# Kernel optimization log

Measured on AMD Instinct MI355X. Metric: run time of the kernel, lower is better.

## Reference

```python
import jax, jax.numpy as jnp
import numpy as np

EPS = 1e-5

def bn(x, gamma, beta, axes):
    # training-mode batchnorm over `axes`, channel axis = 1 (matches nn.BatchNorm1d/2d)
    mean = jnp.mean(x, axis=axes, keepdims=True)
    var = jnp.var(x, axis=axes, keepdims=True)
    shp = [1] * x.ndim
    shp[1] = -1
    return gamma.reshape(shp) * (x - mean) * jax.lax.rsqrt(var + EPS) + beta.reshape(shp)

def setup_inputs():
    key = jax.random.key(0)
    B, N, K, Cin, Cout, m = 4, 4096, 32, 64, 64, 8
    ks = jax.random.split(key, 10)
    def w(k, shape, fan_in):
        return jax.random.normal(k, shape, jnp.float32) * np.float32(np.sqrt(2.0 / fan_in))
    return {
        "x": jax.random.normal(ks[0], (B, Cin, N), jnp.float32),
        "xyz_score": jax.random.normal(ks[1], (B, 66, N, K), jnp.float32),
        "conv1_w": w(ks[2], (Cin, Cin), Cin),
        "bn1_g": jnp.ones((Cin,), jnp.float32), "bn1_b": jnp.zeros((Cin,), jnp.float32),
        "matrice2": w(ks[3], (Cin, m * Cout), Cin),  # weight bank: i x (m*o)
        "sn_w0": w(ks[4], (64, 66), 66), "sn_g0": jnp.ones((64,), jnp.float32), "sn_b0": jnp.zeros((64,), jnp.float32),
        "sn_w1": w(ks[5], (32, 64), 64), "sn_g1": jnp.ones((32,), jnp.float32), "sn_b1": jnp.zeros((32,), jnp.float32),
        "sn_w2": w(ks[6], (16, 32), 32), "sn_g2": jnp.ones((16,), jnp.float32), "sn_b2": jnp.zeros((16,), jnp.float32),
        "sn_w3": w(ks[7], (m, 16), 16), "sn_bias3": jnp.zeros((m,), jnp.float32),
        "bn2_g": jnp.ones((Cout,), jnp.float32), "bn2_b": jnp.zeros((Cout,), jnp.float32),
        "idx": jax.random.randint(ks[8], (B, N, K), 0, N, dtype=jnp.int32),
    }

def reference(x, xyz_score, conv1_w, bn1_g, bn1_b, matrice2,
              sn_w0, sn_g0, sn_b0, sn_w1, sn_g1, sn_b1, sn_w2, sn_g2, sn_b2,
              sn_w3, sn_bias3, bn2_g, bn2_b, idx):
    B, Cin, N = x.shape
    m = sn_w3.shape[0]
    # conv1 (1x1, no bias) + BN1 + ReLU  -> [B, Cin, N]
    h = jnp.einsum('oc,bcn->bon', conv1_w, x)
    h = jax.nn.relu(bn(h, bn1_g, bn1_b, (0, 2)))
    # feat_trans_pointnet: [B,N,Cin] @ [Cin, m*Cout] -> [B,N,m,Cout]
    y = jnp.einsum('bcn,ck->bnk', h, matrice2).reshape(B, N, m, -1)
    # ScoreNet: stack of 1x1 conv2d + BN + ReLU, final conv with bias, softmax over m
    s = xyz_score  # [B, 66, N, K]
    s = jax.nn.relu(bn(jnp.einsum('oc,bcnk->bonk', sn_w0, s), sn_g0, sn_b0, (0, 2, 3)))
    s = jax.nn.relu(bn(jnp.einsum('oc,bcnk->bonk', sn_w1, s), sn_g1, sn_b1, (0, 2, 3)))
    s = jax.nn.relu(bn(jnp.einsum('oc,bcnk->bonk', sn_w2, s), sn_g2, sn_b2, (0, 2, 3)))
    s = jnp.einsum('oc,bcnk->bonk', sn_w3, s) + sn_bias3[None, :, None, None]
    score = jax.nn.softmax(s, axis=1)            # [B, m, N, K], bias=0
    score = jnp.transpose(score, (0, 2, 3, 1))   # [B, N, K, m]
    # assemble_pointnet: gather neighbor transformed feats and score-weight them
    neigh = y[jnp.arange(B)[:, None, None], idx]             # [B, N, K, m, Cout]
    out = jnp.einsum('bnkm,bnkmo->bon', score, neigh)        # [B, Cout, N]
    return jax.nn.relu(bn(out, bn2_g, bn2_b, (0, 2)))
```

## Files before the change

### kernel.cpp

```cpp
#include <hip/hip_runtime.h>
#include <cstdint>

typedef unsigned short u16;
typedef unsigned int   u32;
typedef __attribute__((ext_vector_type(8))) short short8;
typedef __attribute__((ext_vector_type(4))) float f32x4;

constexpr int CB = 4;
constexpr int CN = 4096;
constexpr int CK = 32;
constexpr int NPTS = CB * CN * CK;
constexpr int NBK  = 131072;
constexpr float EPSV = 1e-5f;

struct __align__(16) Q4 { u32 a, b, c, d; };

static __device__ __forceinline__ u16 f2b(float f) {
  union { float f; u32 u; } v; v.f = f;
  u32 u = v.u;
  return (u16)((u + 0x7FFFu + ((u >> 16) & 1u)) >> 16);
}
static __device__ __forceinline__ float b2f(u16 h) {
  union { u32 u; float f; } v; v.u = ((u32)h) << 16;
  return v.f;
}
static __device__ __forceinline__ u32 pk2(float lo, float hi) {
  return (u32)f2b(lo) | ((u32)f2b(hi) << 16);
}
static __device__ __forceinline__ short8 mk8(u32 a, u32 b, u32 c, u32 d) {
  union { u32 w[4]; short8 v; } u; u.w[0]=a; u.w[1]=b; u.w[2]=c; u.w[3]=d; return u.v;
}

__global__ __launch_bounds__(256) void k_conv1(const float* __restrict__ x,
                                               const float* __restrict__ w,
                                               float* __restrict__ h,
                                               float* S, float* Q) {
  __shared__ float wl[64 * 64];
  __shared__ float ls[128];
  int tid = threadIdx.x;
  for (int i = tid; i < 4096; i += 256) wl[i] = w[i];
  if (tid < 128) ls[tid] = 0.f;
  __syncthreads();
  int col = blockIdx.x * 256 + tid;
  int b = col >> 12, n = col & 4095;
  float xr[64];
  const float* xp = x + (size_t)(b * 64) * CN + n;
  #pragma unroll
  for (int c = 0; c < 64; ++c) xr[c] = xp[(size_t)c * CN];
  int lane = tid & 63;
  for (int o = 0; o < 64; ++o) {
    float acc = 0.f;
    const float* wr = &wl[o * 64];
    #pragma unroll
    for (int c = 0; c < 64; ++c) acc = fmaf(wr[c], xr[c], acc);
    h[(size_t)(b * 64 + o) * CN + n] = acc;
    float v = acc, v2 = acc * acc;
    for (int d = 1; d < 64; d <<= 1) { v += __shfl_xor(v, d); v2 += __shfl_xor(v2, d); }
    if (lane == 0) { atomicAdd(&ls[o], v); atomicAdd(&ls[64 + o], v2); }
  }
  __syncthreads();
  if (tid < 64) atomicAdd(&S[tid], ls[tid]);
  else if (tid < 128) atomicAdd(&Q[tid - 64], ls[tid]);
}

__global__ __launch_bounds__(64) void k_affine(const float* S, const float* Q,
                                               const float* g, const float* bt,
                                               float* A, float* Bo, int C, float inv_cnt) {
  int t = threadIdx.x;
  if (t < C) {
    float mean = S[t] * inv_cnt;
    float var = fmaxf(Q[t] * inv_cnt - mean * mean, 0.f);
    float a = g[t] * rsqrtf(var + EPSV);
    A[t] = a;
    Bo[t] = bt[t] - mean * a;
  }
}

__global__ __launch_bounds__(256) void k_y(const float* __restrict__ h,
                                           const float* __restrict__ M2,
                                           const float* __restrict__ Ah,
                                           const float* __restrict__ Bh,
                                           u16* __restrict__ y16) {
  __shared__ float at[64 * 16];
  __shared__ float m2[64 * 128];
  int tid = threadIdx.x;
  int blk = blockIdx.x;
  int b = blk >> 8;
  int n0 = (blk & 255) * 16;
  for (int v = tid; v < 1024; v += 256) {
    int c = v >> 4, nn = v & 15;
    float hv = h[(size_t)(b * 64 + c) * CN + n0 + nn];
    at[v] = fmaxf(fmaf(Ah[c], hv, Bh[c]), 0.f);
  }
  int nn = tid >> 4, k8 = tid & 15;
  for (int ch = 0; ch < 4; ++ch) {
    __syncthreads();
    for (int v = tid; v < 8192; v += 256) {
      int c = v >> 7, kk = v & 127;
      m2[v] = M2[c * 512 + ch * 128 + kk];
    }
    __syncthreads();
    float acc[8] = {0, 0, 0, 0, 0, 0, 0, 0};
    for (int c = 0; c < 64; ++c) {
      float av = at[c * 16 + nn];
      const float* mp = &m2[c * 128 + k8 * 8];
      #pragma unroll
      for (int j = 0; j < 8; ++j) acc[j] = fmaf(av, mp[j], acc[j]);
    }
    u16* yp = &y16[((size_t)(b * CN + n0 + nn)) * 512 + ch * 128 + k8 * 8];
    *(short8*)yp = mk8(pk2(acc[0], acc[1]), pk2(acc[2], acc[3]),
                       pk2(acc[4], acc[5]), pk2(acc[6], acc[7]));
  }
}

static __device__ __forceinline__ void ld_frags(const float* __restrict__ xyz,
                                                int c, int g, int pl, short8 fr[5]) {
  int pbase = c * 32;
  int b = pbase >> 17, r = pbase & (NBK - 1);
  const float* base = xyz + (size_t)b * 66 * NBK + r + g * 8;
  #pragma unroll
  for (int ci = 0; ci < 4; ++ci) {
    const float* p = base + (size_t)(16 * ci + pl) * NBK;
    float4 v0 = *(const float4*)p;
    float4 v1 = *(const float4*)(p + 4);
    fr[ci] = mk8(pk2(v0.x, v0.y), pk2(v0.z, v0.w), pk2(v1.x, v1.y), pk2(v1.z, v1.w));
  }
  if (pl < 2) {
    const float* p = base + (size_t)(64 + pl) * NBK;
    float4 v0 = *(const float4*)p;
    float4 v1 = *(const float4*)(p + 4);
    fr[4] = mk8(pk2(v0.x, v0.y), pk2(v0.z, v0.w), pk2(v1.x, v1.y), pk2(v1.z, v1.w));
  } else if (pl == 2) {
    fr[4] = mk8(0x3F803F80u, 0x3F803F80u, 0x3F803F80u, 0x3F803F80u);
  } else {
    fr[4] = mk8(0u, 0u, 0u, 0u);
  }
}

__global__ __launch_bounds__(256) void k_moment(const float* __restrict__ xyz,
                                                float* __restrict__ Mpart) {
  constexpr int TI[15] = {0,0,0,0,0,1,1,1,1,2,2,2,3,3,4};
  constexpr int TJ[15] = {0,1,2,3,4,1,2,3,4,2,3,4,3,4,4};
  int tid = threadIdx.x;
  int wv = tid >> 6;
  int wid = blockIdx.x * 4 + wv;
  int lane = tid & 63, g = lane >> 4, pl = lane & 15;
  f32x4 acc[15];
  #pragma unroll
  for (int t = 0; t < 15; ++t) acc[t] = (f32x4){0.f, 0.f, 0.f, 0.f};
  for (int cc = wid; cc < NPTS / 32; cc += 4096) {
    short8 fr0[5], fr1[5];
    ld_frags(xyz, cc,        g, pl, fr0);
    ld_frags(xyz, cc + 2048, g, pl, fr1);
    #pragma unroll
    for (int t = 0; t < 15; ++t)
      acc[t] = __builtin_amdgcn_mfma_f32_16x16x32_bf16(fr0[TI[t]], fr0[TJ[t]], acc[t], 0, 0, 0);
    #pragma unroll
    for (int t = 0; t < 15; ++t)
      acc[t] = __builtin_amdgcn_mfma_f32_16x16x32_bf16(fr1[TI[t]], fr1[TJ[t]], acc[t], 0, 0, 0);
  }
  float* mp = Mpart + (size_t)wid * 3840;
  #pragma unroll
  for (int t = 0; t < 15; ++t)
    *(f32x4*)(mp + t * 256 + lane * 4) = acc[t];
}

__global__ __launch_bounds__(256) void k_mreduce(const float* __restrict__ Mpart,
                                                 float* __restrict__ M) {
  int e = blockIdx.x * 256 + threadIdx.x;
  int kg = blockIdx.y;
  float s = 0.f;
  for (int k = kg * 256; k < kg * 256 + 256; ++k) s += Mpart[(size_t)k * 3840 + e];
  atomicAdd(&M[e], s);
}

__global__ __launch_bounds__(256) void k_affine1m(const float* __restrict__ M,
                                                  const float* __restrict__ w0,
                                                  const float* __restrict__ g0,
                                                  const float* __restrict__ b0,
                                                  float* __restrict__ A1,
                                                  float* __restrict__ B1) {
  __shared__ float lsM[67 * 68];
  __shared__ float w0l[64 * 69];
  __shared__ float red[4 * 64];
  int tid = threadIdx.x;
  const float inv = 1.f / (float)NPTS;
  for (int i = tid; i < 67 * 67; i += 256) {
    int r = i / 67, c = i % 67;
    int rr = r, cc = c;
    if ((r >> 4) > (c >> 4)) { rr = c; cc = r; }
    int ti = rr >> 4, tj = cc >> 4;
    int t = ti * (9 - ti) / 2 + tj;
    int rho = rr & 15, kap = cc & 15;
    lsM[r * 68 + c] = M[t * 256 + ((rho >> 2) * 16 + kap) * 4 + (rho & 3)] * inv;
  }
  for (int i = tid; i < 64 * 66; i += 256) {
    int o = i / 66, c = i % 66;
    w0l[o * 69 + c] = w0[i];
  }
  __syncthreads();
  int o = tid & 63, sl = tid >> 6;
  float acc2 = 0.f;
  for (int c1 = sl * 17; c1 < sl * 17 + 17; ++c1) {
    if (c1 >= 66) break;
    float inner = 0.f;
    const float* mr = &lsM[c1 * 68];
    const float* wr = &w0l[o * 69];
    for (int c2 = 0; c2 < 66; ++c2) inner = fmaf(mr[c2], wr[c2], inner);
    acc2 = fmaf(wr[c1], inner, acc2);
  }
  red[sl * 64 + o] = acc2;
  __syncthreads();
  if (sl == 0) {
    float Ez2 = red[o] + red[64 + o] + red[128 + o] + red[192 + o];
    float mean = 0.f;
    const float* wr = &w0l[o * 69];
    for (int c = 0; c < 66; ++c) mean = fmaf(wr[c], lsM[c * 68 + 66], mean);
    float var = fmaxf(Ez2 - mean * mean, 0.f);
    float a = g0[o] * rsqrtf(var + EPSV);
    A1[o] = a;
    B1[o] = b0[o] - mean * a;
  }
}

__global__ __launch_bounds__(256) void k_prep(const float* __restrict__ w0,
                                              const float* __restrict__ w1,
                                              const float* __restrict__ A1,
                                              const float* __restrict__ B1,
                                              u16* __restrict__ w0frag,
                                              u16* __restrict__ w1frag) {
  int tid = threadIdx.x;
  for (int i = tid; i < 6144; i += 256) {
    int e = i & 7, lane = (i >> 3) & 63, t = i >> 9;
    int mt = t / 3, kc = t % 3;
    int row = 16 * mt + (lane & 15);
    int k = 32 * kc + 8 * (lane >> 4) + e;
    float v;
    if (k < 66)      v = A1[row] * w0[row * 66 + k];
    else if (k == 66) v = B1[row];
    else              v = 0.f;
    w0frag[i] = f2b(v);
  }
  for (int i = tid; i < 2048; i += 256) {
    int e = i & 7, lane = (i >> 3) & 63, t = i >> 9;
    int m2t = t >> 1, kc2 = t & 1;
    int row = 16 * m2t + (lane & 15);
    int k = 32 * kc2 + 8 * (lane >> 4) + e;
    w1frag[i] = f2b(w1[row * 64 + k]);
  }
}

__global__ __launch_bounds__(256) void k_s2(const float* __restrict__ xyz,
                                            const u16* __restrict__ w0frag,
                                            const u16* __restrict__ w1frag,
                                            u32* __restrict__ z2p,
                                            float* S, float* Q) {
  __shared__ u16 a1l[4][16][80];
  __shared__ float ls2[64];
  int tid = threadIdx.x;
  int wv = tid >> 6, lane = tid & 63, g = lane >> 4, pl = lane & 15;
  if (tid < 64) ls2[tid] = 0.f;
  __syncthreads();

  const short8* w0f = (const short8*)w0frag;
  const short8* w1f = (const short8*)w1frag;
  short8 A0[4][3];
  #pragma unroll
  for (int mt = 0; mt < 4; ++mt)
    #pragma unroll
    for (int kc = 0; kc < 3; ++kc) A0[mt][kc] = w0f[(mt * 3 + kc) * 64 + lane];
  short8 W1f[2][2];
  #pragma unroll
  for (int m2t = 0; m2t < 2; ++m2t)
    #pragma unroll
    for (int kc2 = 0; kc2 < 2; ++kc2) W1f[m2t][kc2] = w1f[(m2t * 2 + kc2) * 64 + lane];

  float sum8[8], sq8[8];
  #pragma unroll
  for (int i = 0; i < 8; ++i) { sum8[i] = 0.f; sq8[i] = 0.f; }

  int wid = blockIdx.x * 4 + wv;
  for (int s = wid; s < NPTS / 16; s += 8192) {
    int pg = s * 16;
    int b = pg >> 17, r = pg & (NBK - 1);
    const float* sb = xyz + (size_t)b * 66 * NBK + r + pl;
    float v[16];
    #pragma unroll
    for (int e = 0; e < 8; ++e) v[e]     = sb[(size_t)(8 * g + e) * NBK];
    #pragma unroll
    for (int e = 0; e < 8; ++e) v[8 + e] = sb[(size_t)(32 + 8 * g + e) * NBK];
    u32 c2a = 0u, c2b = 0u;
    if (g == 0) {
      float v64 = sb[(size_t)64 * NBK];
      float v65 = sb[(size_t)65 * NBK];
      c2a = pk2(v64, v65);
      c2b = 0x00003F80u;
    }
    short8 Bf0 = mk8(pk2(v[0], v[1]), pk2(v[2], v[3]), pk2(v[4], v[5]), pk2(v[6], v[7]));
    short8 Bf1 = mk8(pk2(v[8], v[9]), pk2(v[10], v[11]), pk2(v[12], v[13]), pk2(v[14], v[15]));
    short8 Bf2 = mk8(c2a, c2b, 0u, 0u);

    #pragma unroll
    for (int mt = 0; mt < 4; ++mt) {
      f32x4 z = {0.f, 0.f, 0.f, 0.f};
      z = __builtin_amdgcn_mfma_f32_16x16x32_bf16(A0[mt][0], Bf0, z, 0, 0, 0);
      z = __builtin_amdgcn_mfma_f32_16x16x32_bf16(A0[mt][1], Bf1, z, 0, 0, 0);
      z = __builtin_amdgcn_mfma_f32_16x16x32_bf16(A0[mt][2], Bf2, z, 0, 0, 0);
      float r0 = fmaxf(z[0], 0.f), r1 = fmaxf(z[1], 0.f);
      float r2 = fmaxf(z[2], 0.f), r3 = fmaxf(z[3], 0.f);
      u32* wp = (u32*)&a1l[wv][pl][16 * mt + 4 * g];
      wp[0] = pk2(r0, r1);
      wp[1] = pk2(r2, r3);
    }
    short8 B2f0 = *(const short8*)&a1l[wv][pl][8 * g];
    short8 B2f1 = *(const short8*)&a1l[wv][pl][32 + 8 * g];
    #pragma unroll
    for (int m2t = 0; m2t < 2; ++m2t) {
      f32x4 z2 = {0.f, 0.f, 0.f, 0.f};
      z2 = __builtin_amdgcn_mfma_f32_16x16x32_bf16(W1f[m2t][0], B2f0, z2, 0, 0, 0);
      z2 = __builtin_amdgcn_mfma_f32_16x16x32_bf16(W1f[m2t][1], B2f1, z2, 0, 0, 0);
      #pragma unroll
      for (int rr = 0; rr < 4; ++rr) {
        sum8[m2t * 4 + rr] += z2[rr];
        sq8[m2t * 4 + rr] += z2[rr] * z2[rr];
      }
      int jlo = 8 * m2t + 2 * g;
      z2p[(size_t)jlo * NPTS + pg + pl]       = pk2(z2[0], z2[1]);
      z2p[(size_t)(jlo + 1) * NPTS + pg + pl] = pk2(z2[2], z2[3]);
    }
  }
  #pragma unroll
  for (int i = 0; i < 8; ++i) {
    float vS = sum8[i], vQ = sq8[i];
    for (int d = 1; d < 16; d <<= 1) { vS += __shfl_xor(vS, d); vQ += __shfl_xor(vQ, d); }
    if (pl == 0) {
      int ch = 16 * (i >> 2) + 4 * g + (i & 3);
      atomicAdd(&ls2[ch], vS);
      atomicAdd(&ls2[32 + ch], vQ);
    }
  }
  __syncthreads();
  if (tid < 32) atomicAdd(&S[tid], ls2[tid]);
  else if (tid < 64) atomicAdd(&Q[tid - 32], ls2[tid]);
}

__global__ __launch_bounds__(256) void k_s3(const u32* __restrict__ z2p,
                                            const float* __restrict__ w2,
                                            const float* __restrict__ A2,
                                            const float* __restrict__ B2,
                                            u32* __restrict__ z3,
                                            float* S, float* Q) {
  __shared__ float w2l[16 * 32];
  __shared__ float ab[64];
  __shared__ float ls[32];
  int tid = threadIdx.x;
  for (int i = tid; i < 512; i += 256) w2l[i] = w2[i];
  if (tid < 32) { ab[tid] = A2[tid]; ls[tid] = 0.f; }
  else if (tid < 64) ab[tid] = B2[tid - 32];
  __syncthreads();
  int p = blockIdx.x * 256 + tid;
  float a2[32];
  #pragma unroll
  for (int j = 0; j < 16; ++j) {
    u32 wj = z2p[(size_t)j * NPTS + p];
    float lo = b2f((u16)(wj & 0xFFFFu));
    float hi = b2f((u16)(wj >> 16));
    a2[2 * j]     = fmaxf(fmaf(ab[2 * j], lo, ab[32 + 2 * j]), 0.f);
    a2[2 * j + 1] = fmaxf(fmaf(ab[2 * j + 1], hi, ab[32 + 2 * j + 1]), 0.f);
  }
  int lane = tid & 63;
  float zt[16];
  for (int j = 0; j < 16; ++j) {
    float z = 0.f;
    const float* wr = &w2l[j * 32];
    #pragma unroll
    for (int c = 0; c < 32; ++c) z = fmaf(wr[c], a2[c], z);
    zt[j] = z;
    float v = z, v2 = z * z;
    for (int d = 1; d < 64; d <<= 1) { v += __shfl_xor(v, d); v2 += __shfl_xor(v2, d); }
    if (lane == 0) { atomicAdd(&ls[j], v); atomicAdd(&ls[16 + j], v2); }
  }
  u32 pkk[8];
  #pragma unroll
  for (int j = 0; j < 8; ++j) pkk[j] = pk2(zt[2 * j], zt[2 * j + 1]);
  Q4* dst = (Q4*)(z3 + (size_t)p * 8);
  #pragma unroll
  for (int i = 0; i < 2; ++i) { Q4 q; q.a = pkk[4*i]; q.b = pkk[4*i+1]; q.c = pkk[4*i+2]; q.d = pkk[4*i+3]; dst[i] = q; }
  __syncthreads();
  if (tid < 16) atomicAdd(&S[tid], ls[tid]);
  else if (tid < 32) atomicAdd(&Q[tid - 16], ls[tid]);
}

__global__ __launch_bounds__(256) void k_score(const u32* __restrict__ z3,
                                               const float* __restrict__ w3,
                                               const float* __restrict__ bias3,
                                               const float* __restrict__ A3,
                                               const float* __restrict__ B3,
                                               float* __restrict__ scores) {
  __shared__ float w3l[128];
  __shared__ float bl[8];
  __shared__ float ab[32];
  int tid = threadIdx.x;
  if (tid < 128) w3l[tid] = w3[tid];
  if (tid < 8) bl[tid] = bias3[tid];
  if (tid < 16) ab[tid] = A3[tid];
  else if (tid < 32) ab[tid] = B3[tid - 16];
  __syncthreads();
  int p = blockIdx.x * 256 + tid;
  const Q4* zp = (const Q4*)(z3 + (size_t)p * 8);
  Q4 r0 = zp[0], r1 = zp[1];
  u32 w8[8] = {r0.a, r0.b, r0.c, r0.d, r1.a, r1.b, r1.c, r1.d};
  float a3[16];
  #pragma unroll
  for (int t = 0; t < 8; ++t) {
    int c = t * 2;
    a3[c]     = fmaxf(fmaf(ab[c], b2f((u16)(w8[t] & 0xFFFFu)), ab[16 + c]), 0.f);
    a3[c + 1] = fmaxf(fmaf(ab[c + 1], b2f((u16)(w8[t] >> 16)), ab[16 + c + 1]), 0.f);
  }
  float z4[8]; float mx = -1e30f;
  #pragma unroll
  for (int mI = 0; mI < 8; ++mI) {
    float z = bl[mI];
    const float* wr = &w3l[mI * 16];
    #pragma unroll
    for (int c = 0; c < 16; ++c) z = fmaf(wr[c], a3[c], z);
    z4[mI] = z; mx = fmaxf(mx, z);
  }
  float ssum = 0.f;
  #pragma unroll
  for (int mI = 0; mI < 8; ++mI) { z4[mI] = __expf(z4[mI] - mx); ssum += z4[mI]; }
  float inv = 1.f / ssum;
  float4* sp = (float4*)(scores + (size_t)p * 8);
  sp[0] = make_float4(z4[0] * inv, z4[1] * inv, z4[2] * inv, z4[3] * inv);
  sp[1] = make_float4(z4[4] * inv, z4[5] * inv, z4[6] * inv, z4[7] * inv);
}

__global__ __launch_bounds__(256) void k_gather(const u16* __restrict__ y16,
                                                const float* __restrict__ scores,
                                                const int* __restrict__ idx,
                                                float* __restrict__ out0,
                                                float* S, float* Q) {
  __shared__ float ls[128];
  int tid = threadIdx.x;
  if (tid < 128) ls[tid] = 0.f;
  __syncthreads();
  int bid = blockIdx.x;
  int batch = (bid & 7) >> 1;
  int sub = ((bid >> 3) << 1) | (bid & 1);
  int wv = tid >> 6, lane = tid & 63;
  int m = lane >> 3, og = lane & 7;
  const u16* ybase = y16 + (size_t)batch * CN * 512;
  for (int i = 0; i < 2; ++i) {
    int pid = (batch << 12) + sub * 8 + wv * 2 + i;
    int pbase = pid * 32;
    float acc8[8] = {0, 0, 0, 0, 0, 0, 0, 0};
    for (int k = 0; k < 32; ++k) {
      int p = pbase + k;
      int j = idx[p];
      float s = scores[(size_t)p * 8 + m];
      short8 yv = *(const short8*)(ybase + ((size_t)j << 9) + lane * 8);
      #pragma unroll
      for (int t = 0; t < 8; ++t)
        acc8[t] = fmaf(s, b2f((u16)yv[t]), acc8[t]);
    }
    #pragma unroll
    for (int d = 8; d < 64; d <<= 1) {
      #pragma unroll
      for (int t = 0; t < 8; ++t) acc8[t] += __shfl_xor(acc8[t], d);
    }
    if (m == 0) {
      float* op = out0 + (size_t)pid * 64 + og * 8;
      *(float4*)op       = make_float4(acc8[0], acc8[1], acc8[2], acc8[3]);
      *(float4*)(op + 4) = make_float4(acc8[4], acc8[5], acc8[6], acc8[7]);
      #pragma unroll
      for (int t = 0; t < 8; ++t) {
        atomicAdd(&ls[og * 8 + t], acc8[t]);
        atomicAdd(&ls[64 + og * 8 + t], acc8[t] * acc8[t]);
      }
    }
  }
  __syncthreads();
  if (tid < 64) atomicAdd(&S[tid], ls[tid]);
  else if (tid < 128) atomicAdd(&Q[tid - 64], ls[tid]);
}

__global__ __launch_bounds__(256) void k_bn2(const float* __restrict__ out0,
                                             const float* __restrict__ A,
                                             const float* __restrict__ Bo,
                                             float* __restrict__ outp) {
  int gid = blockIdx.x * 256 + threadIdx.x;
  for (int i = gid; i < CB * 64 * CN; i += 262144) {
    int b = i >> 18, o = (i >> 12) & 63, n = i & 4095;
    float v = out0[((size_t)((b << 12) | n)) * 64 + o];
    outp[i] = fmaxf(fmaf(A[o], v, Bo[o]), 0.f);
  }
}

extern "C" void kernel_launch(void* const* d_in, const int* in_sizes, int n_in,
                              void* d_out, int out_size, void* d_ws, size_t ws_size,
                              hipStream_t stream) {
  const float* x       = (const float*)d_in[0];
  const float* xyz     = (const float*)d_in[1];
  const float* conv1_w = (const float*)d_in[2];
  const float* bn1_g   = (const float*)d_in[3];
  const float* bn1_b   = (const float*)d_in[4];
  const float* M2      = (const float*)d_in[5];
  const float* w0      = (const float*)d_in[6];
  const float* g0      = (const float*)d_in[7];
  const float* b0      = (const float*)d_in[8];
  const float* w1      = (const float*)d_in[9];
  const float* g1      = (const float*)d_in[10];
  const float* b1      = (const float*)d_in[11];
  const float* w2      = (const float*)d_in[12];
  const float* g2      = (const float*)d_in[13];
  const float* b2      = (const float*)d_in[14];
  const float* w3      = (const float*)d_in[15];
  const float* bias3   = (const float*)d_in[16];
  const float* bn2_g   = (const float*)d_in[17];
  const float* bn2_b   = (const float*)d_in[18];
  const int*   idx     = (const int*)d_in[19];
  float* out = (float*)d_out;

  char* wsb = (char*)d_ws;
  float* h      = (float*)wsb;
  u16*   y16    = (u16*)(wsb + 4194304);
  float* scores = (float*)(wsb + 20971520);
  u32*   z2p    = (u32*)(wsb + 37748736);
  u32*   z3     = (u32*)(wsb + 71303168);
  float* out0   = (float*)(wsb + 88080384);
  float* sums   = (float*)(wsb + 92274688);
  float* S_h = sums;        float* Q_h = sums + 64;
  float* S_2 = sums + 128;  float* Q_2 = sums + 160;
  float* S_3 = sums + 192;  float* Q_3 = sums + 208;
  float* S_o = sums + 224;  float* Q_o = sums + 288;
  float* Mm  = sums + 352;
  float* A_h = sums + 6752; float* B_h = sums + 6816;
  float* A_1 = sums + 6880; float* B_1 = sums + 6944;
  float* A_2 = sums + 7008; float* B_2 = sums + 7040;
  float* A_3 = sums + 7072; float* B_3 = sums + 7088;
  float* A_o = sums + 7104; float* B_o = sums + 7168;
  u16* w0frag = (u16*)(sums + 7232);
  u16* w1frag = w0frag + 6144;
  float* Mpart = (float*)z2p;

  hipMemsetAsync(sums, 0, 6752 * sizeof(float), stream);

  k_conv1<<<64, 256, 0, stream>>>(x, conv1_w, h, S_h, Q_h);
  k_affine<<<1, 64, 0, stream>>>(S_h, Q_h, bn1_g, bn1_b, A_h, B_h, 64, 1.f / 16384.f);
  k_y<<<1024, 256, 0, stream>>>(h, M2, A_h, B_h, y16);

  k_moment<<<512, 256, 0, stream>>>(xyz, Mpart);
  k_mreduce<<<dim3(15, 8), 256, 0, stream>>>(Mpart, Mm);
  k_affine1m<<<1, 256, 0, stream>>>(Mm, w0, g0, b0, A_1, B_1);
  k_prep<<<1, 256, 0, stream>>>(w0, w1, A_1, B_1, w0frag, w1frag);
  k_s2<<<2048, 256, 0, stream>>>(xyz, w0frag, w1frag, z2p, S_2, Q_2);
  k_affine<<<1, 64, 0, stream>>>(S_2, Q_2, g1, b1, A_2, B_2, 32, 1.f / (float)NPTS);
  k_s3<<<2048, 256, 0, stream>>>(z2p, w2, A_2, B_2, z3, S_3, Q_3);
  k_affine<<<1, 64, 0, stream>>>(S_3, Q_3, g2, b2, A_3, B_3, 16, 1.f / (float)NPTS);

  k_score<<<2048, 256, 0, stream>>>(z3, w3, bias3, A_3, B_3, scores);
  k_gather<<<2048, 256, 0, stream>>>(y16, scores, idx, out0, S_o, Q_o);
  k_affine<<<1, 64, 0, stream>>>(S_o, Q_o, bn2_g, bn2_b, A_o, B_o, 64, 1.f / 16384.f);
  k_bn2<<<1024, 256, 0, stream>>>(out0, A_o, B_o, out);
}
```

Measured before the change: 379.9 us.

## Compute feature transform y with bf16 MFMA using prepacked M2 fragments

Replaces the scalar-FMA k_y kernel, which reloaded a 64x128 M2 chunk into shared memory four times per block, with a wave-level bf16 MFMA (16x16x32) implementation. A new k_prepM2 kernel converts M2 once into MFMA A-fragment layout in bf16. Each wave computes 16 points x 512 outputs, stages the results in padded LDS and writes them out as coalesced rows. This trades fp32 accumulation of bf16-rounded inputs for matrix-core throughput and adds one small extra launch.

```diff
diff --git a/kernel.cpp b/kernel.cpp
--- a/kernel.cpp
+++ b/kernel.cpp
@@ -76,40 +76,62 @@
   }
 }
 
+__global__ __launch_bounds__(256) void k_prepM2(const float* __restrict__ M2,
+                                                u16* __restrict__ m2frag) {
+  int i = blockIdx.x * 256 + threadIdx.x;
+  int e = i & 7, lane = (i >> 3) & 63, t = i >> 9;
+  int mt = t >> 1, kc = t & 1;
+  int row = 16 * mt + (lane & 15);
+  int k = 32 * kc + 8 * (lane >> 4) + e;
+  m2frag[i] = f2b(M2[k * 512 + row]);
+}
+
 __global__ __launch_bounds__(256) void k_y(const float* __restrict__ h,
-                                           const float* __restrict__ M2,
+                                           const u16* __restrict__ m2frag,
                                            const float* __restrict__ Ah,
                                            const float* __restrict__ Bh,
                                            u16* __restrict__ y16) {
-  __shared__ float at[64 * 16];
-  __shared__ float m2[64 * 128];
-  int tid = threadIdx.x;
-  int blk = blockIdx.x;
-  int b = blk >> 8;
-  int n0 = (blk & 255) * 16;
-  for (int v = tid; v < 1024; v += 256) {
-    int c = v >> 4, nn = v & 15;
-    float hv = h[(size_t)(b * 64 + c) * CN + n0 + nn];
-    at[v] = fmaxf(fmaf(Ah[c], hv, Bh[c]), 0.f);
-  }
-  int nn = tid >> 4, k8 = tid & 15;
-  for (int ch = 0; ch < 4; ++ch) {
-    __syncthreads();
-    for (int v = tid; v < 8192; v += 256) {
-      int c = v >> 7, kk = v & 127;
-      m2[v] = M2[c * 512 + ch * 128 + kk];
-    }
-    __syncthreads();
-    float acc[8] = {0, 0, 0, 0, 0, 0, 0, 0};
-    for (int c = 0; c < 64; ++c) {
-      float av = at[c * 16 + nn];
-      const float* mp = &m2[c * 128 + k8 * 8];
-      #pragma unroll
-      for (int j = 0; j < 8; ++j) acc[j] = fmaf(av, mp[j], acc[j]);
-    }
-    u16* yp = &y16[((size_t)(b * CN + n0 + nn)) * 512 + ch * 128 + k8 * 8];
-    *(short8*)yp = mk8(pk2(acc[0], acc[1]), pk2(acc[2], acc[3]),
-                       pk2(acc[4], acc[5]), pk2(acc[6], acc[7]));
+  __shared__ u16 yl[4][16 * 520];
+  __shared__ float abl[128];
+  int tid = threadIdx.x;
+  if (tid < 64) abl[tid] = Ah[tid];
+  else if (tid < 128) abl[tid] = Bh[tid - 64];
+  int wv = tid >> 6, lane = tid & 63, g = lane >> 4, pl = lane & 15;
+  __syncthreads();
+  int wid = blockIdx.x * 4 + wv;
+  int n0 = wid * 16;
+  int b = n0 >> 12, nloc = n0 & 4095;
+  const float* sb = h + (size_t)(b * 64) * CN + nloc + pl;
+  u32 w[8];
+  #pragma unroll
+  for (int kc = 0; kc < 2; ++kc) {
+    #pragma unroll
+    for (int e2 = 0; e2 < 4; ++e2) {
+      int c0 = 32 * kc + 8 * g + 2 * e2;
+      float v0 = fmaxf(fmaf(abl[c0],     sb[(size_t)c0 * CN],       abl[64 + c0]),     0.f);
+      float v1 = fmaxf(fmaf(abl[c0 + 1], sb[(size_t)(c0 + 1) * CN], abl[64 + c0 + 1]), 0.f);
+      w[kc * 4 + e2] = pk2(v0, v1);
+    }
+  }
+  short8 Bf0 = mk8(w[0], w[1], w[2], w[3]);
+  short8 Bf1 = mk8(w[4], w[5], w[6], w[7]);
+  const short8* m2f = (const short8*)m2frag;
+  u16* ylw = &yl[wv][0];
+  #pragma unroll
+  for (int mt = 0; mt < 32; ++mt) {
+    short8 A0 = m2f[(mt * 2 + 0) * 64 + lane];
+    short8 A1 = m2f[(mt * 2 + 1) * 64 + lane];
+    f32x4 z = {0.f, 0.f, 0.f, 0.f};
+    z = __builtin_amdgcn_mfma_f32_16x16x32_bf16(A0, Bf0, z, 0, 0, 0);
+    z = __builtin_amdgcn_mfma_f32_16x16x32_bf16(A1, Bf1, z, 0, 0, 0);
+    u32* wp = (u32*)&ylw[pl * 520 + 16 * mt + 4 * g];
+    wp[0] = pk2(z[0], z[1]);
+    wp[1] = pk2(z[2], z[3]);
+  }
+  u16* yg = y16 + (size_t)n0 * 512;
+  for (int j = 0; j < 16; ++j) {
+    short8 v = *(const short8*)&ylw[j * 520 + lane * 8];
+    *(short8*)(yg + (size_t)j * 512 + lane * 8) = v;
   }
 }
 
@@ -541,13 +563,15 @@
   float* A_o = sums + 7104; float* B_o = sums + 7168;
   u16* w0frag = (u16*)(sums + 7232);
   u16* w1frag = w0frag + 6144;
+  u16* m2frag = w1frag + 2048;
   float* Mpart = (float*)z2p;
 
   hipMemsetAsync(sums, 0, 6752 * sizeof(float), stream);
 
+  k_prepM2<<<128, 256, 0, stream>>>(M2, m2frag);
   k_conv1<<<64, 256, 0, stream>>>(x, conv1_w, h, S_h, Q_h);
   k_affine<<<1, 64, 0, stream>>>(S_h, Q_h, bn1_g, bn1_b, A_h, B_h, 64, 1.f / 16384.f);
-  k_y<<<1024, 256, 0, stream>>>(h, M2, A_h, B_h, y16);
+  k_y<<<256, 256, 0, stream>>>(h, m2frag, A_h, B_h, y16);
 
   k_moment<<<512, 256, 0, stream>>>(xyz, Mpart);
   k_mreduce<<<dim3(15, 8), 256, 0, stream>>>(Mpart, Mm);
```

New measurement: 345.1 us. 9.2% less time.
